# Kernel optimization log

Hardware: AMD Instinct MI355X
Metric: run time of the kernel (lower is better)

The kernel has to match this reference:

```python
import jax, jax.numpy as jnp
import numpy as np

HIGHWAY_BIAS = 0.0
# SRU rescale=True scales the highway residual to preserve variance:
# scale_x = sqrt(1 + exp(2*highway_bias)) = sqrt(2) for highway_bias=0
SCALE_X = float(np.sqrt(1.0 + np.exp(2.0 * HIGHWAY_BIAS)))
D = 128  # SRU hidden size


def sru_layer(x, W, v, b):
    """One SRU layer. x: (T,B,din); W: (din,k*D) with k=4 if din!=D else 3;
    v: (2,D) recurrent gate weights; b: (2,D) gate biases."""
    T, B, din = x.shape
    k = W.shape[1] // D
    U = jnp.einsum('tbi,ij->tbj', x, W).reshape(T, B, k, D)
    u0, u1, u2 = U[:, :, 0], U[:, :, 1], U[:, :, 2]
    res = U[:, :, 3] if k == 4 else x  # highway residual (projected if dims differ)
    vf, vr = v[0], v[1]
    bf, br = b[0], b[1]

    def step(c, inp):
        u0t, u1t, u2t, rt = inp
        f = jax.nn.sigmoid(u1t + vf * c + bf)          # forget gate (peeks at c_{t-1})
        c_new = f * c + (1.0 - f) * u0t                # cell update
        r = jax.nn.sigmoid(u2t + vr * c_new + br)      # reset/highway gate
        h = r * c_new + (1.0 - r) * rt * SCALE_X       # highway output
        return c_new, h

    c0 = jnp.zeros((B, D), x.dtype)
    _, h = jax.lax.scan(step, c0, (u0, u1, u2, res))
    return h  # (T,B,D)


def sru_stack(x, W0, v0, b0, W1, v1, b1):
    return sru_layer(sru_layer(x, W0, v0, b0), W1, v1, b1)


def setup_inputs() -> dict:
    key = jax.random.key(0)
    ks = jax.random.split(key, 20)
    B, T = 8, 32000
    s_in = 1.0 / np.sqrt(64.0)
    s_hid = 1.0 / np.sqrt(128.0)
    inp = {
        'tensor': jax.random.normal(ks[0], (B, 9, T), jnp.float32),
        'W_first': jax.random.normal(ks[1], (128, 9), jnp.float32) / 3.0,
        'b_first': jnp.zeros((128,), jnp.float32),
        'W_last': jax.random.normal(ks[2], (1, 128), jnp.float32) * s_hid,
        'b_last': jnp.zeros((1,), jnp.float32),
        # stack a = self.lstm2 (processes channels [:64])
        'a_W0': jax.random.normal(ks[3], (64, 4 * D), jnp.float32) * s_in,
        'a_v0': jax.random.normal(ks[4], (2, D), jnp.float32) * 0.1,
        'a_b0': jnp.zeros((2, D), jnp.float32),
        'a_W1': jax.random.normal(ks[5], (D, 3 * D), jnp.float32) * s_hid,
        'a_v1': jax.random.normal(ks[6], (2, D), jnp.float32) * 0.1,
        'a_b1': jnp.zeros((2, D), jnp.float32),
        # stack b = self.lstm (processes channels [64:])
        'b_W0': jax.random.normal(ks[7], (64, 4 * D), jnp.float32) * s_in,
        'b_v0': jax.random.normal(ks[8], (2, D), jnp.float32) * 0.1,
        'b_b0': jnp.zeros((2, D), jnp.float32),
        'b_W1': jax.random.normal(ks[9], (D, 3 * D), jnp.float32) * s_hid,
        'b_v1': jax.random.normal(ks[10], (2, D), jnp.float32) * 0.1,
        'b_b1': jnp.zeros((2, D), jnp.float32),
    }
    return inp


def reference(tensor, W_first, b_first, W_last, b_last,
              a_W0, a_v0, a_b0, a_W1, a_v1, a_b1,
              b_W0, b_v0, b_b0, b_W1, b_v1, b_b1):
    # first: Conv1d(9,128,1)
    h = jnp.einsum('oc,bct->bot', W_first, tensor) + b_first[None, :, None]  # (B,128,T)
    xa = jnp.transpose(h[:, :64], (2, 0, 1))   # (T,B,64) -> lstm2
    xb = jnp.transpose(h[:, 64:], (2, 0, 1))   # (T,B,64) -> lstm
    ya = sru_stack(xa, a_W0, a_v0, a_b0, a_W1, a_v1, a_b1)  # (T,B,128)
    yb = sru_stack(xb, b_W0, b_v0, b_b0, b_W1, b_v1, b_b1)
    s = jnp.transpose(ya + yb, (1, 2, 0))      # (B,128,T)
    # last: Conv1d(128,1,1)
    return jnp.einsum('oc,bct->bot', W_last, s) + b_last[None, :, None]  # (B,1,T)
```

## Files before the change

### kernel.cpp

```cpp
#include <hip/hip_runtime.h>
#include <hip/hip_bf16.h>

#define L2E   1.44269504088896340736f
#define SQRT2 1.41421356237309504880f

#define T_LEN 32000
#define BATCH 8
#define NCH   9

#define KCH0  64
#define CL0   500
#define WU    128
#define KCH1  32
#define CL1   1000
#define WUF   136
#define NTIL  71

#define MROWS (T_LEN*BATCH)

typedef __bf16 bf16x8 __attribute__((ext_vector_type(8)));
typedef float  f32x4  __attribute__((ext_vector_type(4)));
typedef float  f32x2  __attribute__((ext_vector_type(2)));

__global__ void prep_misc(const float* __restrict__ Wf, const float* __restrict__ bfirst,
                          const float* __restrict__ aW0, const float* __restrict__ bW0,
                          const float* __restrict__ ab0, const float* __restrict__ bb0,
                          const float* __restrict__ ab1, const float* __restrict__ bb1,
                          float* __restrict__ Mn, float* __restrict__ biasn,
                          float* __restrict__ bias1n) {
    int s = blockIdx.x, g = blockIdx.y;
    int d = threadIdx.x;
    const float* W0s = s ? bW0 : aW0;
    const float* b0s = s ? bb0 : ab0;
    const float* b1s = s ? bb1 : ab1;

    float scale = (g == 1 || g == 2) ? -L2E : (g == 3 ? SQRT2 : 1.0f);
    float bias = 0.f;
    for (int i = 0; i < 64; ++i) bias += bfirst[s*64 + i] * W0s[i*512 + g*128 + d];
    for (int c = 0; c < NCH; ++c) {
        float acc = 0.f;
        for (int i = 0; i < 64; ++i)
            acc += Wf[(s*64 + i)*NCH + c] * W0s[i*512 + g*128 + d];
        Mn[((s*NCH + c)*4 + g)*128 + d] = scale * acc;
    }
    float bb = bias;
    if (g == 1) bb = bias + b0s[d];
    if (g == 2) bb = bias + b0s[128 + d];
    biasn[(s*4 + g)*128 + d] = scale * bb;

    if (g == 0) {
        bias1n[s*384 + d      ] = 0.0f;
        bias1n[s*384 + 128 + d] = -L2E * b1s[d];
        bias1n[s*384 + 256 + d] = -L2E * b1s[128 + d];
    }
}

__global__ void prep_bpack(const float* __restrict__ aW1, const float* __restrict__ bW1,
                           __hip_bfloat16* __restrict__ Bpack) {
    int nt = blockIdx.x, s = blockIdx.y;
    int kt = threadIdx.x >> 6, lane = threadIdx.x & 63;
    const float* W1s = s ? bW1 : aW1;
    int n = nt*16 + (lane & 15);
    float csc = (n < 128) ? 1.0f : -L2E;
    for (int jj = 0; jj < 8; ++jj) {
        int k = kt*32 + (lane >> 4)*8 + jj;
        Bpack[((size_t)((s*24 + nt)*4 + kt)*64 + lane)*8 + jj] =
            __float2bfloat16(csc * W1s[k*384 + n]);
    }
}

__global__ __launch_bounds__(256) void scan0(const float* __restrict__ tensor,
        const float* __restrict__ av0, const float* __restrict__ bv0,
        const float* __restrict__ Mn, const float* __restrict__ biasn,
        __hip_bfloat16* __restrict__ h0) {
    __shared__ __align__(16) float ldsx[(CL0 + WU) * 12];
    int chunk = blockIdx.x, b = blockIdx.y;
    int tid = threadIdx.x, wid = tid >> 6, lane = tid & 63;
    int s = wid >> 1, half = wid & 1, d = half*64 + lane;

    int t0 = chunk*CL0 - WU; if (t0 < 0) t0 = 0;
    int tend = (chunk + 1)*CL0;
    int nsteps = tend - t0;

    for (int c = 0; c < NCH; ++c) {
        const float* src = tensor + ((size_t)b*NCH + c)*T_LEN + t0;
        for (int j = tid; j < nsteps; j += 256) ldsx[j*12 + c] = src[j];
    }
    __syncthreads();

    f32x2 M01[NCH], M23[NCH], b01, b23;
    {
        float M[4][NCH], bi[4];
#pragma unroll
        for (int g = 0; g < 4; ++g) {
            bi[g] = biasn[(s*4 + g)*128 + d];
#pragma unroll
            for (int c = 0; c < NCH; ++c) M[g][c] = Mn[((s*NCH + c)*4 + g)*128 + d];
        }
#pragma unroll
        for (int c = 0; c < NCH; ++c) {
            M01[c] = (f32x2){M[0][c], M[1][c]};
            M23[c] = (f32x2){M[2][c], M[3][c]};
        }
        b01 = (f32x2){bi[0], bi[1]};
        b23 = (f32x2){bi[2], bi[3]};
    }
    const float* v0s = s ? bv0 : av0;
    float vf2 = -L2E * v0s[d];
    float vr2 = -L2E * v0s[128 + d];

    float cst = 0.f;
    int hw_off = chunk*CL0 - t0;
    __hip_bfloat16* hbase = h0 + ((size_t)s*MROWS + b)*128 + d;

    auto compU = [&](int grp, f32x2* u01v, f32x2* u23v) {
#pragma unroll
        for (int k = 0; k < 4; ++k) {
            const float* xr = ldsx + (grp*4 + k)*12;
            float4 xlo = *(const float4*)xr;
            float4 xhi = *(const float4*)(xr + 4);
            float x8 = xr[8];
            f32x2 a = b01, c2 = b23;
            a += M01[0]*xlo.x; c2 += M23[0]*xlo.x;
            a += M01[1]*xlo.y; c2 += M23[1]*xlo.y;
            a += M01[2]*xlo.z; c2 += M23[2]*xlo.z;
            a += M01[3]*xlo.w; c2 += M23[3]*xlo.w;
            a += M01[4]*xhi.x; c2 += M23[4]*xhi.x;
            a += M01[5]*xhi.y; c2 += M23[5]*xhi.y;
            a += M01[6]*xhi.z; c2 += M23[6]*xhi.z;
            a += M01[7]*xhi.w; c2 += M23[7]*xhi.w;
            a += M01[8]*x8;    c2 += M23[8]*x8;
            u01v[k] = a; u23v[k] = c2;
        }
    };
    auto chain = [&](f32x2* u01v, f32x2* u23v, int grp) {
#pragma unroll
        for (int k = 0; k < 4; ++k) {
            float e  = __builtin_amdgcn_exp2f(fmaf(vf2, cst, u01v[k].y));
            float cn = __builtin_amdgcn_rcpf(e + 1.0f) * fmaf(e, u01v[k].x, cst);
            float er = __builtin_amdgcn_exp2f(fmaf(vr2, cn, u23v[k].x));
            float rr = __builtin_amdgcn_rcpf(er + 1.0f);
            float h  = fmaf(rr, cn - u23v[k].y, u23v[k].y);
            cst = cn;
            int j = grp*4 + k;
            if (j >= hw_off) hbase[(size_t)(t0 + j)*(BATCH*128)] = __float2bfloat16(h);
        }
    };

    f32x2 uA01[4], uA23[4], uB01[4], uB23[4];
    int ngrp = nsteps >> 2;
    compU(0, uA01, uA23);
    int g = 0;
    while (g + 2 <= ngrp) {
        compU(g + 1, uB01, uB23);
        chain(uA01, uA23, g);
        if (g + 2 < ngrp) compU(g + 2, uA01, uA23);
        chain(uB01, uB23, g + 1);
        g += 2;
    }
    if (g < ngrp) chain(uA01, uA23, g);
}

__global__ __launch_bounds__(512) void scan1f(const __hip_bfloat16* __restrict__ h0,
        const __hip_bfloat16* __restrict__ Bpack, const float* __restrict__ bias1n,
        const float* __restrict__ av1, const float* __restrict__ bv1,
        const float* __restrict__ Wlast, float* __restrict__ pbuf) {
    __shared__ __align__(16) float ush[2*16*388];
    int chunk = blockIdx.x, b = blockIdx.y;
    int tid = threadIdx.x, wid = tid >> 6, lane = tid & 63;
    int s_g = wid >> 2, ntb = (wid & 3)*6, cl = lane & 15, rsel = lane >> 4;
    int tw = chunk*CL1, t0 = tw - WUF;

    bf16x8 Bfr[6][4];
    const bf16x8* bsrc = (const bf16x8*)Bpack;
#pragma unroll
    for (int i = 0; i < 6; ++i)
#pragma unroll
        for (int kt = 0; kt < 4; ++kt)
            Bfr[i][kt] = bsrc[((s_g*24 + ntb + i)*4 + kt)*64 + lane];
    float bias[6];
#pragma unroll
    for (int i = 0; i < 6; ++i) bias[i] = bias1n[s_g*384 + (ntb + i)*16 + cl];

    int s_s = wid >> 1, half = wid & 1, d = half*64 + lane;
    const float* v1s = (s_s & 1) ? bv1 : av1;
    float vf2 = -L2E * v1s[d], vr2 = -L2E * v1s[128 + d];
    float wl = Wlast[d];
    float cst = 0.f;
    float* pb = pbuf + ((size_t)(wid & 3)*BATCH + b)*T_LEN;
    const __hip_bfloat16* hres = h0 + ((size_t)(s_s & 1)*MROWS + b)*128 + d;
    const __hip_bfloat16* habase = h0 + ((size_t)s_g*MROWS + b)*128;

    auto loadA = [&](int tile, bf16x8* A) {
        int trow = t0 + tile*16 + cl; if (trow < 0) trow = 0;
        const __hip_bfloat16* ap = habase + (size_t)trow*(BATCH*128) + rsel*8;
#pragma unroll
        for (int kt = 0; kt < 4; ++kt) A[kt] = *(const bf16x8*)(ap + kt*32);
    };
    auto loadR = [&](int tile, float* rv) {
#pragma unroll
        for (int k = 0; k < 16; ++k) {
            int t = t0 + tile*16 + k; if (t < 0) t = 0;
            rv[k] = __bfloat162float(hres[(size_t)t*(BATCH*128)]);
        }
    };

    bf16x8 Afr[4], Afrn[4];
    float resv[16], resn[16];
    loadA(0, Afr);
    if (wid < 4) loadR(0, resv);

    for (int tile = 0; tile < NTIL; ++tile) {
        int tt0 = t0 + tile*16;

        f32x4 acc[6];
#pragma unroll
        for (int i = 0; i < 6; ++i) acc[i] = (f32x4){bias[i], bias[i], bias[i], bias[i]};
#pragma unroll
        for (int kt = 0; kt < 4; ++kt)
#pragma unroll
            for (int i = 0; i < 6; ++i)
                acc[i] = __builtin_amdgcn_mfma_f32_16x16x32_bf16(Afr[kt], Bfr[i][kt], acc[i], 0, 0, 0);

        __syncthreads();
#pragma unroll
        for (int i = 0; i < 6; ++i) {
            int col = (ntb + i)*16 + cl;
#pragma unroll
            for (int j = 0; j < 4; ++j)
                ush[(s_g*16 + rsel*4 + j)*388 + col] = acc[i][j];
        }

        int tnext = (tile + 1 < NTIL) ? tile + 1 : tile;
        loadA(tnext, Afrn);
        if (wid < 4) loadR(tnext, resn);

        __syncthreads();

        if (wid < 4) {
#pragma unroll
            for (int sub = 0; sub < 2; ++sub) {
                float u0v[8], u1v[8], u2v[8], hv[8];
#pragma unroll
                for (int k = 0; k < 8; ++k) {
                    const float* ur = ush + (s_s*16 + sub*8 + k)*388;
                    u0v[k] = ur[d]; u1v[k] = ur[128 + d]; u2v[k] = ur[256 + d];
                }
#pragma unroll
                for (int k = 0; k < 8; ++k) {
                    int t = tt0 + sub*8 + k;
                    float e  = __builtin_amdgcn_exp2f(fmaf(vf2, cst, u1v[k]));
                    float cn = __builtin_amdgcn_rcpf(e + 1.0f) * fmaf(e, u0v[k], cst);
                    float er = __builtin_amdgcn_exp2f(fmaf(vr2, cn, u2v[k]));
                    float rr = __builtin_amdgcn_rcpf(er + 1.0f);
                    float sr = SQRT2 * resv[sub*8 + k];
                    hv[k] = fmaf(rr, cn - sr, sr);
                    cst = (t >= 0) ? cn : cst;
                }
                float sel = 0.f;
#pragma unroll
                for (int k = 0; k < 8; ++k) {
                    float p = wl * hv[k];
#pragma unroll
                    for (int m = 32; m >= 1; m >>= 1) p += __shfl_xor(p, m);
                    if (lane == k) sel = p;
                }
                int tsel = tt0 + sub*8 + lane;
                if (lane < 8 && tsel >= tw) pb[tsel] = sel;
            }
        }
#pragma unroll
        for (int kt = 0; kt < 4; ++kt) Afr[kt] = Afrn[kt];
        if (wid < 4) {
#pragma unroll
            for (int k = 0; k < 16; ++k) resv[k] = resn[k];
        }
    }
}

__global__ void finalk(const float* __restrict__ pbuf, const float* __restrict__ blast,
                       float* __restrict__ out) {
    int idx = blockIdx.x*256 + threadIdx.x;
    if (idx >= BATCH*T_LEN) return;
    int b = idx / T_LEN, t = idx - b*T_LEN;
    float v = blast[0];
#pragma unroll
    for (int k = 0; k < 4; ++k) v += pbuf[((size_t)k*BATCH + b)*T_LEN + t];
    out[idx] = v;
}

extern "C" void kernel_launch(void* const* d_in, const int* in_sizes, int n_in,
                              void* d_out, int out_size, void* d_ws, size_t ws_size,
                              hipStream_t stream) {
    const float* tensor = (const float*)d_in[0];
    const float* Wfirst = (const float*)d_in[1];
    const float* bfirst = (const float*)d_in[2];
    const float* Wlast  = (const float*)d_in[3];
    const float* blast  = (const float*)d_in[4];
    const float* aW0 = (const float*)d_in[5];
    const float* av0 = (const float*)d_in[6];
    const float* ab0 = (const float*)d_in[7];
    const float* aW1 = (const float*)d_in[8];
    const float* av1 = (const float*)d_in[9];
    const float* ab1 = (const float*)d_in[10];
    const float* bW0 = (const float*)d_in[11];
    const float* bv0 = (const float*)d_in[12];
    const float* bb0 = (const float*)d_in[13];
    const float* bW1 = (const float*)d_in[14];
    const float* bv1 = (const float*)d_in[15];
    const float* bb1 = (const float*)d_in[16];
    float* out = (float*)d_out;

    char* ws = (char*)d_ws;
    size_t off = 0;
    float* Mn     = (float*)(ws + off); off += 2*9*4*128*sizeof(float);
    float* biasn  = (float*)(ws + off); off += 2*4*128*sizeof(float);
    float* bias1n = (float*)(ws + off); off += 2*384*sizeof(float);
    off = (off + 255) & ~(size_t)255;
    __hip_bfloat16* Bpack = (__hip_bfloat16*)(ws + off); off += (size_t)2*24*4*64*8*2;
    off = (off + 255) & ~(size_t)255;
    float* pbuf = (float*)(ws + off); off += (size_t)4*BATCH*T_LEN*sizeof(float);
    off = (off + 255) & ~(size_t)255;
    __hip_bfloat16* h0 = (__hip_bfloat16*)(ws + off); off += (size_t)2*MROWS*128*2;
    (void)ws_size; (void)in_sizes; (void)n_in; (void)out_size;

    prep_misc<<<dim3(2, 4), 128, 0, stream>>>(Wfirst, bfirst, aW0, bW0, ab0, bb0, ab1, bb1,
                                              Mn, biasn, bias1n);
    prep_bpack<<<dim3(24, 2), 256, 0, stream>>>(aW1, bW1, Bpack);
    scan0<<<dim3(KCH0, BATCH), 256, 0, stream>>>(tensor, av0, bv0, Mn, biasn, h0);
    scan1f<<<dim3(KCH1, BATCH), 512, 0, stream>>>(h0, Bpack, bias1n, av1, bv1, Wlast, pbuf);
    finalk<<<dim3((BATCH*T_LEN + 255)/256), 256, 0, stream>>>(pbuf, blast, out);
}
```

Measured before the change: 480.6 us.

## Warp-specialize scan1f into producer GEMM and consumer scan waves with double buffering

scan1f now runs 12 waves: 8 producer waves compute the MFMA projection one tile ahead into double-buffered LDS and stage the residual h0 values there, while 4 consumer waves run the serial recurrence. This takes the GEMM and the global residual loads off the recurrence's critical path. The consumer also uses a cheaper two-stage shuffle reduction and folds warm-up masking into u1 = -inf. Separately, scan0 gets shorter chunks (more blocks) with an occupancy hint, and the cell update is rewritten as a single fma. Costs are more LDS per block and more threads per block; the scan0 tail-group handling was removed, which relies on the new chunk length dividing evenly.

```diff
diff --git a/kernel.cpp b/kernel.cpp
--- a/kernel.cpp
+++ b/kernel.cpp
@@ -8,8 +8,8 @@
 #define BATCH 8
 #define NCH   9
 
-#define KCH0  64
-#define CL0   500
+#define KCH0  125
+#define CL0   256
 #define WU    128
 #define KCH1  32
 #define CL1   1000
@@ -69,7 +69,7 @@
     }
 }
 
-__global__ __launch_bounds__(256) void scan0(const float* __restrict__ tensor,
+__global__ __launch_bounds__(256, 4) void scan0(const float* __restrict__ tensor,
         const float* __restrict__ av0, const float* __restrict__ bv0,
         const float* __restrict__ Mn, const float* __restrict__ biasn,
         __hip_bfloat16* __restrict__ h0) {
@@ -137,7 +137,8 @@
 #pragma unroll
         for (int k = 0; k < 4; ++k) {
             float e  = __builtin_amdgcn_exp2f(fmaf(vf2, cst, u01v[k].y));
-            float cn = __builtin_amdgcn_rcpf(e + 1.0f) * fmaf(e, u01v[k].x, cst);
+            float g  = __builtin_amdgcn_rcpf(e + 1.0f);
+            float cn = fmaf(g, cst - u01v[k].x, u01v[k].x);
             float er = __builtin_amdgcn_exp2f(fmaf(vr2, cn, u23v[k].x));
             float rr = __builtin_amdgcn_rcpf(er + 1.0f);
             float h  = fmaf(rr, cn - u23v[k].y, u23v[k].y);
@@ -158,122 +159,144 @@
         chain(uB01, uB23, g + 1);
         g += 2;
     }
-    if (g < ngrp) chain(uA01, uA23, g);
-}
-
-__global__ __launch_bounds__(512) void scan1f(const __hip_bfloat16* __restrict__ h0,
+}
+
+__global__ __launch_bounds__(768, 3) void scan1f(const __hip_bfloat16* __restrict__ h0,
         const __hip_bfloat16* __restrict__ Bpack, const float* __restrict__ bias1n,
         const float* __restrict__ av1, const float* __restrict__ bv1,
         const float* __restrict__ Wlast, float* __restrict__ pbuf) {
-    __shared__ __align__(16) float ush[2*16*388];
+    __shared__ __align__(16) float ush[2][2][16][388];
+    __shared__ unsigned int hstg[2][2][16][64];
     int chunk = blockIdx.x, b = blockIdx.y;
     int tid = threadIdx.x, wid = tid >> 6, lane = tid & 63;
-    int s_g = wid >> 2, ntb = (wid & 3)*6, cl = lane & 15, rsel = lane >> 4;
+    int cl = lane & 15, rsel = lane >> 4;
     int tw = chunk*CL1, t0 = tw - WUF;
-
-    bf16x8 Bfr[6][4];
-    const bf16x8* bsrc = (const bf16x8*)Bpack;
-#pragma unroll
-    for (int i = 0; i < 6; ++i)
-#pragma unroll
-        for (int kt = 0; kt < 4; ++kt)
-            Bfr[i][kt] = bsrc[((s_g*24 + ntb + i)*4 + kt)*64 + lane];
-    float bias[6];
-#pragma unroll
-    for (int i = 0; i < 6; ++i) bias[i] = bias1n[s_g*384 + (ntb + i)*16 + cl];
-
-    int s_s = wid >> 1, half = wid & 1, d = half*64 + lane;
-    const float* v1s = (s_s & 1) ? bv1 : av1;
-    float vf2 = -L2E * v1s[d], vr2 = -L2E * v1s[128 + d];
-    float wl = Wlast[d];
-    float cst = 0.f;
-    float* pb = pbuf + ((size_t)(wid & 3)*BATCH + b)*T_LEN;
-    const __hip_bfloat16* hres = h0 + ((size_t)(s_s & 1)*MROWS + b)*128 + d;
-    const __hip_bfloat16* habase = h0 + ((size_t)s_g*MROWS + b)*128;
-
-    auto loadA = [&](int tile, bf16x8* A) {
-        int trow = t0 + tile*16 + cl; if (trow < 0) trow = 0;
-        const __hip_bfloat16* ap = habase + (size_t)trow*(BATCH*128) + rsel*8;
-#pragma unroll
-        for (int kt = 0; kt < 4; ++kt) A[kt] = *(const bf16x8*)(ap + kt*32);
-    };
-    auto loadR = [&](int tile, float* rv) {
-#pragma unroll
-        for (int k = 0; k < 16; ++k) {
-            int t = t0 + tile*16 + k; if (t < 0) t = 0;
-            rv[k] = __bfloat162float(hres[(size_t)t*(BATCH*128)]);
-        }
-    };
-
-    bf16x8 Afr[4], Afrn[4];
-    float resv[16], resn[16];
-    loadA(0, Afr);
-    if (wid < 4) loadR(0, resv);
-
-    for (int tile = 0; tile < NTIL; ++tile) {
-        int tt0 = t0 + tile*16;
-
-        f32x4 acc[6];
-#pragma unroll
-        for (int i = 0; i < 6; ++i) acc[i] = (f32x4){bias[i], bias[i], bias[i], bias[i]};
-#pragma unroll
-        for (int kt = 0; kt < 4; ++kt)
-#pragma unroll
-            for (int i = 0; i < 6; ++i)
-                acc[i] = __builtin_amdgcn_mfma_f32_16x16x32_bf16(Afr[kt], Bfr[i][kt], acc[i], 0, 0, 0);
-
-        __syncthreads();
-#pragma unroll
-        for (int i = 0; i < 6; ++i) {
-            int col = (ntb + i)*16 + cl;
-#pragma unroll
-            for (int j = 0; j < 4; ++j)
-                ush[(s_g*16 + rsel*4 + j)*388 + col] = acc[i][j];
-        }
-
-        int tnext = (tile + 1 < NTIL) ? tile + 1 : tile;
-        loadA(tnext, Afrn);
-        if (wid < 4) loadR(tnext, resn);
-
-        __syncthreads();
-
-        if (wid < 4) {
-#pragma unroll
-            for (int sub = 0; sub < 2; ++sub) {
-                float u0v[8], u1v[8], u2v[8], hv[8];
+    int pp = 0;
+
+    if (wid >= 4) {
+        int gw = wid - 4;
+        int s_g = gw >> 2;
+        int ntb = (gw & 3) * 6;
+        bool hwr = ((gw & 3) == 0);
+        bf16x8 Bfr[6][4];
+        const bf16x8* bsrc = (const bf16x8*)Bpack;
+#pragma unroll
+        for (int i = 0; i < 6; ++i)
+#pragma unroll
+            for (int kt = 0; kt < 4; ++kt)
+                Bfr[i][kt] = bsrc[((s_g*24 + ntb + i)*4 + kt)*64 + lane];
+        float bias[6];
+#pragma unroll
+        for (int i = 0; i < 6; ++i) bias[i] = bias1n[s_g*384 + (ntb + i)*16 + cl];
+
+        const __hip_bfloat16* habase = h0 + ((size_t)s_g*MROWS + b)*128 + rsel*8;
+        bf16x8 A[4];
+        auto loadA = [&](int tile) {
+            int trow = t0 + tile*16 + cl; if (trow < 0) trow = 0;
+            const __hip_bfloat16* ap = habase + (size_t)trow*(BATCH*128);
+#pragma unroll
+            for (int kt = 0; kt < 4; ++kt) A[kt] = *(const bf16x8*)(ap + kt*32);
+        };
+        auto gemmwrite = [&](int ppw) {
+            f32x4 acc[6];
+#pragma unroll
+            for (int i = 0; i < 6; ++i) acc[i] = (f32x4){bias[i], bias[i], bias[i], bias[i]};
+#pragma unroll
+            for (int kt = 0; kt < 4; ++kt)
+#pragma unroll
+                for (int i = 0; i < 6; ++i)
+                    acc[i] = __builtin_amdgcn_mfma_f32_16x16x32_bf16(A[kt], Bfr[i][kt], acc[i], 0, 0, 0);
+            if (hwr) {
+#pragma unroll
+                for (int kt = 0; kt < 4; ++kt) {
+                    uint4 aw = __builtin_bit_cast(uint4, A[kt]);
+                    unsigned int* hrow = &hstg[ppw][s_g][cl][0];
+                    hrow[(rsel*4 + kt*16 + 0) ^ cl] = aw.x;
+                    hrow[(rsel*4 + kt*16 + 1) ^ cl] = aw.y;
+                    hrow[(rsel*4 + kt*16 + 2) ^ cl] = aw.z;
+                    hrow[(rsel*4 + kt*16 + 3) ^ cl] = aw.w;
+                }
+            }
+#pragma unroll
+            for (int i = 0; i < 6; ++i) {
+                int col = (ntb + i)*16 + cl;
+#pragma unroll
+                for (int j = 0; j < 4; ++j)
+                    ush[ppw][s_g][rsel*4 + j][col] = acc[i][j];
+            }
+        };
+        loadA(0);
+        gemmwrite(0);
+        loadA(1);
+        for (int tile = 0; tile < NTIL; ++tile) {
+            __syncthreads();
+            if (tile + 1 < NTIL) {
+                gemmwrite(pp ^ 1);
+                int tn = tile + 2; if (tn > NTIL - 1) tn = NTIL - 1;
+                loadA(tn);
+            }
+            pp ^= 1;
+        }
+    } else {
+        int s_s = wid >> 1, half = wid & 1, d = half*64 + lane;
+        const float* v1s = s_s ? bv1 : av1;
+        float vf2 = -L2E * v1s[d], vr2 = -L2E * v1s[128 + d];
+        float wl = Wlast[d];
+        float cst = 0.f;
+        float* pb = pbuf + ((size_t)wid*BATCH + b)*T_LEN;
+        int dsw = d >> 1, dodd = lane & 1;
+
+        for (int tile = 0; tile < NTIL; ++tile) {
+            __syncthreads();
+            int tt0 = t0 + tile*16;
+#pragma unroll
+            for (int h8 = 0; h8 < 2; ++h8) {
+                float u0v[8], u1v[8], u2v[8], rv[8], hv[8];
 #pragma unroll
                 for (int k = 0; k < 8; ++k) {
-                    const float* ur = ush + (s_s*16 + sub*8 + k)*388;
+                    int tt = h8*8 + k;
+                    const float* ur = &ush[pp][s_s][tt][0];
                     u0v[k] = ur[d]; u1v[k] = ur[128 + d]; u2v[k] = ur[256 + d];
+                    unsigned int w = hstg[pp][s_s][tt][dsw ^ tt];
+                    unsigned int hb = dodd ? (w >> 16) : (w & 0xffffu);
+                    rv[k] = __uint_as_float(hb << 16);
+                    if (tt0 + tt < 0) u1v[k] = -__builtin_inff();
                 }
 #pragma unroll
                 for (int k = 0; k < 8; ++k) {
-                    int t = tt0 + sub*8 + k;
                     float e  = __builtin_amdgcn_exp2f(fmaf(vf2, cst, u1v[k]));
-                    float cn = __builtin_amdgcn_rcpf(e + 1.0f) * fmaf(e, u0v[k], cst);
+                    float g  = __builtin_amdgcn_rcpf(e + 1.0f);
+                    float cn = fmaf(g, cst - u0v[k], u0v[k]);
                     float er = __builtin_amdgcn_exp2f(fmaf(vr2, cn, u2v[k]));
                     float rr = __builtin_amdgcn_rcpf(er + 1.0f);
-                    float sr = SQRT2 * resv[sub*8 + k];
+                    float sr = SQRT2 * rv[k];
                     hv[k] = fmaf(rr, cn - sr, sr);
-                    cst = (t >= 0) ? cn : cst;
+                    cst = cn;
                 }
-                float sel = 0.f;
+                float pr[8];
 #pragma unroll
                 for (int k = 0; k < 8; ++k) {
                     float p = wl * hv[k];
-#pragma unroll
-                    for (int m = 32; m >= 1; m >>= 1) p += __shfl_xor(p, m);
-                    if (lane == k) sel = p;
+                    p += __shfl_xor(p, 32);
+                    p += __shfl_xor(p, 16);
+                    p += __shfl_xor(p, 8);
+                    pr[k] = p;
                 }
-                int tsel = tt0 + sub*8 + lane;
-                if (lane < 8 && tsel >= tw) pb[tsel] = sel;
+                int g3 = lane >> 3;
+                float a0 = (g3 & 1) ? pr[1] : pr[0];
+                float a1 = (g3 & 1) ? pr[3] : pr[2];
+                float a2 = (g3 & 1) ? pr[5] : pr[4];
+                float a3 = (g3 & 1) ? pr[7] : pr[6];
+                float b0 = (g3 & 2) ? a1 : a0;
+                float b1 = (g3 & 2) ? a3 : a2;
+                float q  = (g3 & 4) ? b1 : b0;
+                q += __shfl_xor(q, 1);
+                q += __shfl_xor(q, 2);
+                q += __shfl_xor(q, 4);
+                int tsel = tt0 + h8*8 + g3;
+                if ((lane & 7) == 0 && tsel >= tw) pb[tsel] = q;
             }
-        }
-#pragma unroll
-        for (int kt = 0; kt < 4; ++kt) Afr[kt] = Afrn[kt];
-        if (wid < 4) {
-#pragma unroll
-            for (int k = 0; k < 16; ++k) resv[k] = resn[k];
+            pp ^= 1;
         }
     }
 }
@@ -328,6 +351,6 @@
                                               Mn, biasn, bias1n);
     prep_bpack<<<dim3(24, 2), 256, 0, stream>>>(aW1, bW1, Bpack);
     scan0<<<dim3(KCH0, BATCH), 256, 0, stream>>>(tensor, av0, bv0, Mn, biasn, h0);
-    scan1f<<<dim3(KCH1, BATCH), 512, 0, stream>>>(h0, Bpack, bias1n, av1, bv1, Wlast, pbuf);
+    scan1f<<<dim3(KCH1, BATCH), 768, 0, stream>>>(h0, Bpack, bias1n, av1, bv1, Wlast, pbuf);
     finalk<<<dim3((BATCH*T_LEN + 255)/256), 256, 0, stream>>>(pbuf, blast, out);
 }
```

After: 457.3 us. 1.05x faster.
